# Kernel optimization log

Measured on AMD Instinct MI355X. Metric: run time of the kernel, lower is better.

## Reference

```python
import jax, jax.numpy as jnp
import numpy as np

INPUT_DIM = 256
OUTPUT_DIM = 256
DEGREE = 7


def setup_inputs() -> dict:
    key = jax.random.key(0)
    k1, k2 = jax.random.split(key)
    x = jax.random.normal(k1, (16, 2048, INPUT_DIM), dtype=jnp.float32)
    std = 1.0 / (INPUT_DIM * (DEGREE + 1))
    hermite_coeffs = std * jax.random.normal(k2, (INPUT_DIM, OUTPUT_DIM, DEGREE + 1), dtype=jnp.float32)
    return {"x": x, "hermite_coeffs": hermite_coeffs}


def reference(x, hermite_coeffs):
    a, b, c = x.shape
    degree = hermite_coeffs.shape[2] - 1
    xf = jnp.tanh(x.reshape(-1, c))  # [N, input_dim]
    hs = [jnp.ones_like(xf)]
    if degree > 0:
        hs.append(2.0 * xf)
    for i in range(2, degree + 1):
        hs.append(2.0 * xf * hs[-1] - 2.0 * (i - 1) * hs[-2])
    hermite = jnp.stack(hs, axis=-1)  # [N, input_dim, degree+1]
    y = jnp.einsum('bid,iod->bo', hermite, hermite_coeffs)
    return y.reshape(a, b, hermite_coeffs.shape[1])
```

## Files before the change

### kernel.cpp

```cpp
#include <hip/hip_runtime.h>
#include <hip/hip_bf16.h>
#include <math.h>

#define INPUT_DIM 256
#define OUT_DIM   256
#define NDEG      8
#define KTOT      (INPUT_DIM * NDEG)
#define NROWS     (16 * 2048)

#define BM  64
#define BN  128
#define BK  64
#define NK  (KTOT / BK)
#define LDT 72
#define CHUNK_ELEMS 8192

typedef __bf16 bf16x8 __attribute__((ext_vector_type(8)));
typedef float  f32x4  __attribute__((ext_vector_type(4)));

__global__ __launch_bounds__(256) void reorder_coeffs(const float* __restrict__ C,
                                                      __bf16* __restrict__ Bt) {
    int g = blockIdx.x * 256 + threadIdx.x;
    int i = g >> 8;
    int o = g & 255;
    const float4* src = (const float4*)(C + (size_t)i * (OUT_DIM * NDEG) + o * NDEG);
    float4 a = src[0];
    float4 b = src[1];
    bf16x8 v;
    v[0] = (__bf16)a.x; v[1] = (__bf16)a.y; v[2] = (__bf16)a.z; v[3] = (__bf16)a.w;
    v[4] = (__bf16)b.x; v[5] = (__bf16)b.y; v[6] = (__bf16)b.z; v[7] = (__bf16)b.w;
    int bn = o >> 7;
    int ol = o & 127;
    int kc = i >> 3;
    int p  = i & 7;
    size_t dst = (size_t)(bn * 32 + kc) * CHUNK_ELEMS + p * 1024 + ol * 8;
    *(bf16x8*)(Bt + dst) = v;
}

__global__ __launch_bounds__(256, 4) void hermite_mfma(const float* __restrict__ x,
                                                       const __bf16* __restrict__ Bt,
                                                       float* __restrict__ out) {
    __shared__ __align__(16) __bf16 Alds[BM * LDT];
    __shared__ __align__(16) __bf16 Blds[CHUNK_ELEMS];

    const int tid  = threadIdx.x;
    const int bm   = blockIdx.x;
    const int bn   = blockIdx.y;
    const int wave = tid >> 6;
    const int lane = tid & 63;
    const int wr   = (wave >> 1) * 32;
    const int wc   = (wave & 1) * 64;
    const int lrow = lane & 15;
    const int quad = lane >> 4;

    const int am = tid >> 2;
    const int ah = (tid & 3) * 2;
    const float* xrow = x + (size_t)(bm * BM + am) * INPUT_DIM + ah;

    const __bf16* chunk0 = Bt + (size_t)bn * 32 * CHUNK_ELEMS;
    const int woff = wave * 2048 + lane * 8;

    f32x4 acc[2][4] = {};

    for (int kc = 0; kc < NK; ++kc) {
        float2 xv = *(const float2*)(xrow + kc * 8);

        const __bf16* gsrc = chunk0 + (size_t)kc * CHUNK_ELEMS + woff;
        #pragma unroll
        for (int i = 0; i < 4; ++i) {
            __builtin_amdgcn_global_load_lds(
                (const __attribute__((address_space(1))) void*)(gsrc + i * 512),
                (__attribute__((address_space(3))) void*)(&Blds[wave * 2048 + i * 512 + lane * 8]),
                16, 0, 0);
        }

        #pragma unroll
        for (int j = 0; j < 2; ++j) {
            float xs = (&xv.x)[j];
            float e = __expf(2.0f * xs);
            float t = 1.0f - 2.0f / (e + 1.0f);
            bf16x8 v;
            float hm2 = 1.0f;
            float hm1 = 2.0f * t;
            v[0] = (__bf16)hm2;
            v[1] = (__bf16)hm1;
            #pragma unroll
            for (int d = 2; d < 8; ++d) {
                float h = 2.0f * t * hm1 - 2.0f * (float)(d - 1) * hm2;
                v[d] = (__bf16)h;
                hm2 = hm1; hm1 = h;
            }
            *(bf16x8*)(&Alds[am * LDT + (ah + j) * 8]) = v;
        }

        __syncthreads();

        #pragma unroll
        for (int ki = 0; ki < 2; ++ki) {
            bf16x8 af[2], bfr[4];
            #pragma unroll
            for (int mi = 0; mi < 2; ++mi)
                af[mi] = *(const bf16x8*)(&Alds[(wr + mi * 16 + lrow) * LDT + ki * 32 + quad * 8]);
            #pragma unroll
            for (int ni = 0; ni < 4; ++ni)
                bfr[ni] = *(const bf16x8*)(&Blds[((ki * 4 + quad) * 128 + (wc + ni * 16 + lrow)) * 8]);
            #pragma unroll
            for (int mi = 0; mi < 2; ++mi)
                #pragma unroll
                for (int ni = 0; ni < 4; ++ni)
                    acc[mi][ni] = __builtin_amdgcn_mfma_f32_16x16x32_bf16(
                        af[mi], bfr[ni], acc[mi][ni], 0, 0, 0);
        }

        __syncthreads();
    }

    #pragma unroll
    for (int mi = 0; mi < 2; ++mi) {
        #pragma unroll
        for (int r = 0; r < 4; ++r) {
            int row = bm * BM + wr + mi * 16 + quad * 4 + r;
            float* orow = out + (size_t)row * OUT_DIM + bn * BN + wc + lrow;
            #pragma unroll
            for (int ni = 0; ni < 4; ++ni)
                orow[ni * 16] = acc[mi][ni][r];
        }
    }
}

extern "C" void kernel_launch(void* const* d_in, const int* in_sizes, int n_in,
                              void* d_out, int out_size, void* d_ws, size_t ws_size,
                              hipStream_t stream) {
    const float* x = (const float*)d_in[0];
    const float* C = (const float*)d_in[1];
    float* out = (float*)d_out;
    __bf16* Bt = (__bf16*)d_ws;

    reorder_coeffs<<<dim3((INPUT_DIM * OUT_DIM) / 256), dim3(256), 0, stream>>>(C, Bt);
    hermite_mfma<<<dim3(NROWS / BM, OUT_DIM / BN), dim3(256), 0, stream>>>(x, Bt, out);
}
```

Baseline: 123.9 us.

## Widen output tile to full 256 columns with 512-thread blocks

Each block now covers all 256 output columns using 8 waves, so every block computes the Hermite features of its 64 rows once instead of once per column tile. The coefficient layout is changed to match, with one contiguous 16K-element chunk per k-step. This removes the duplicated tanh/recurrence work and the repeated x reads across column tiles. In exchange the grid has half as many blocks and each block uses more LDS per stage, which can lower occupancy.

Result: no change. 121.6 us (-1.8%).

```diff
diff --git a/kernel.cpp b/kernel.cpp
--- a/kernel.cpp
+++ b/kernel.cpp
@@ -9,11 +9,11 @@
 #define NROWS     (16 * 2048)
 
 #define BM  64
-#define BN  128
+#define BN  256
 #define BK  64
 #define NK  (KTOT / BK)
 #define LDT 72
-#define CHUNK_ELEMS 8192
+#define CHUNK_ELEMS 16384
 
 typedef __bf16 bf16x8 __attribute__((ext_vector_type(8)));
 typedef float  f32x4  __attribute__((ext_vector_type(4)));
@@ -29,15 +29,13 @@
     bf16x8 v;
     v[0] = (__bf16)a.x; v[1] = (__bf16)a.y; v[2] = (__bf16)a.z; v[3] = (__bf16)a.w;
     v[4] = (__bf16)b.x; v[5] = (__bf16)b.y; v[6] = (__bf16)b.z; v[7] = (__bf16)b.w;
-    int bn = o >> 7;
-    int ol = o & 127;
     int kc = i >> 3;
     int p  = i & 7;
-    size_t dst = (size_t)(bn * 32 + kc) * CHUNK_ELEMS + p * 1024 + ol * 8;
+    size_t dst = (size_t)kc * CHUNK_ELEMS + p * 2048 + o * 8;
     *(bf16x8*)(Bt + dst) = v;
 }
 
-__global__ __launch_bounds__(256, 4) void hermite_mfma(const float* __restrict__ x,
+__global__ __launch_bounds__(512, 4) void hermite_mfma(const float* __restrict__ x,
                                                        const __bf16* __restrict__ Bt,
                                                        float* __restrict__ out) {
     __shared__ __align__(16) __bf16 Alds[BM * LDT];
@@ -45,38 +43,34 @@
 
     const int tid  = threadIdx.x;
     const int bm   = blockIdx.x;
-    const int bn   = blockIdx.y;
     const int wave = tid >> 6;
     const int lane = tid & 63;
-    const int wr   = (wave >> 1) * 32;
-    const int wc   = (wave & 1) * 64;
+    const int wr   = (wave >> 2) * 32;
+    const int wc   = (wave & 3) * 64;
     const int lrow = lane & 15;
     const int quad = lane >> 4;
 
-    const int am = tid >> 2;
-    const int ah = (tid & 3) * 2;
-    const float* xrow = x + (size_t)(bm * BM + am) * INPUT_DIM + ah;
+    const int am = tid >> 3;
+    const int ah = tid & 7;
+    const float* xptr = x + (size_t)(bm * BM + am) * INPUT_DIM + ah;
 
-    const __bf16* chunk0 = Bt + (size_t)bn * 32 * CHUNK_ELEMS;
-    const int woff = wave * 2048 + lane * 8;
+    const int wbase = wave * 2048 + lane * 8;
 
     f32x4 acc[2][4] = {};
 
     for (int kc = 0; kc < NK; ++kc) {
-        float2 xv = *(const float2*)(xrow + kc * 8);
+        float xs = xptr[kc * 8];
 
-        const __bf16* gsrc = chunk0 + (size_t)kc * CHUNK_ELEMS + woff;
+        const __bf16* gsrc = Bt + (size_t)kc * CHUNK_ELEMS + wbase;
         #pragma unroll
         for (int i = 0; i < 4; ++i) {
             __builtin_amdgcn_global_load_lds(
                 (const __attribute__((address_space(1))) void*)(gsrc + i * 512),
-                (__attribute__((address_space(3))) void*)(&Blds[wave * 2048 + i * 512 + lane * 8]),
+                (__attribute__((address_space(3))) void*)(&Blds[wbase + i * 512]),
                 16, 0, 0);
         }
 
-        #pragma unroll
-        for (int j = 0; j < 2; ++j) {
-            float xs = (&xv.x)[j];
+        {
             float e = __expf(2.0f * xs);
             float t = 1.0f - 2.0f / (e + 1.0f);
             bf16x8 v;
@@ -90,7 +84,7 @@
                 v[d] = (__bf16)h;
                 hm2 = hm1; hm1 = h;
             }
-            *(bf16x8*)(&Alds[am * LDT + (ah + j) * 8]) = v;
+            *(bf16x8*)(&Alds[am * LDT + ah * 8]) = v;
         }
 
         __syncthreads();
@@ -103,7 +97,7 @@
                 af[mi] = *(const bf16x8*)(&Alds[(wr + mi * 16 + lrow) * LDT + ki * 32 + quad * 8]);
             #pragma unroll
             for (int ni = 0; ni < 4; ++ni)
-                bfr[ni] = *(const bf16x8*)(&Blds[((ki * 4 + quad) * 128 + (wc + ni * 16 + lrow)) * 8]);
+                bfr[ni] = *(const bf16x8*)(&Blds[(ki * 4 + quad) * 2048 + (wc + ni * 16 + lrow) * 8]);
             #pragma unroll
             for (int mi = 0; mi < 2; ++mi)
                 #pragma unroll
@@ -120,7 +114,7 @@
         #pragma unroll
         for (int r = 0; r < 4; ++r) {
             int row = bm * BM + wr + mi * 16 + quad * 4 + r;
-            float* orow = out + (size_t)row * OUT_DIM + bn * BN + wc + lrow;
+            float* orow = out + (size_t)row * OUT_DIM + wc + lrow;
             #pragma unroll
             for (int ni = 0; ni < 4; ++ni)
                 orow[ni * 16] = acc[mi][ni][r];
@@ -137,5 +131,5 @@
     __bf16* Bt = (__bf16*)d_ws;
 
     reorder_coeffs<<<dim3((INPUT_DIM * OUT_DIM) / 256), dim3(256), 0, stream>>>(C, Bt);
-    hermite_mfma<<<dim3(NROWS / BM, OUT_DIM / BN), dim3(256), 0, stream>>>(x, Bt, out);
+    hermite_mfma<<<dim3(NROWS / BM), dim3(512), 0, stream>>>(x, Bt, out);
 }
```
